# Kernel tuning notes

Hardware: AMD Instinct MI355X
Metric: run time of the kernel (lower is better)

The kernel has to match this reference:

```python
import jax, jax.numpy as jnp
import numpy as np

T, B, D, H = 512, 256, 256, 256  # seq_len, batch, input_dim, hidden_dim == n_qubits


def setup_inputs() -> dict:
    key = jax.random.key(0)
    k1, k2, k3 = jax.random.split(key, 3)
    inputs = jax.random.normal(k1, (T, B, D), dtype=jnp.float32)
    # stacked gate linears: order [forget, input, update, output]
    W = jax.random.normal(k2, (4, H, D + H), dtype=jnp.float32) * 0.05
    b = jax.random.normal(k3, (4, H), dtype=jnp.float32) * 0.05
    return {"inputs": inputs, "W": W, "b": b}


def reference(inputs, W, b):
    # Quantum gate with mean_field=True reduces exactly to cos(.):
    # |0> --RX(x)--> <Z> = cos(x); RZ layers are diagonal in Z and leave <Z> unchanged.
    batch = inputs.shape[1]
    h0 = jnp.zeros((batch, H), dtype=inputs.dtype)
    c0 = jnp.zeros((batch, H), dtype=inputs.dtype)

    def step(carry, x_t):
        h, c = carry
        comb = jnp.concatenate([x_t, h], axis=1)            # [B, D+H]
        z = jnp.einsum('gqd,bd->gbq', W, comb) + b[:, None, :]  # [4, B, H]
        f = jax.nn.sigmoid(jnp.cos(z[0]))
        i = jax.nn.sigmoid(jnp.cos(z[1]))
        g = jnp.tanh(jnp.cos(z[2]))
        o = jax.nn.sigmoid(jnp.cos(z[3]))
        c_new = f * c + i * g
        h_new = o * jnp.tanh(c_new)
        return (h_new, c_new), h_new

    (h_last, c_last), outputs = jax.lax.scan(step, (h0, c0), inputs)
    return outputs, h_last, c_last
```

## Files before the change

### kernel.cpp

```cpp
#include <hip/hip_runtime.h>

#define T_ 512
#define B_ 256
#define D_ 256
#define H_ 256

typedef short s16x8 __attribute__((ext_vector_type(8)));
typedef float f32x4 __attribute__((ext_vector_type(4)));

static __device__ __forceinline__ unsigned short f2bf(float f){
  unsigned u = __float_as_uint(f);
  u += 0x7FFFu + ((u >> 16) & 1u);
  return (unsigned short)(u >> 16);
}
static __device__ __forceinline__ float bf2f(unsigned short h){
  return __uint_as_float(((unsigned)h) << 16);
}
static __device__ __forceinline__ unsigned pk2(float a, float b){
  return (unsigned)f2bf(a) | ((unsigned)f2bf(b) << 16);
}
static __device__ __forceinline__ float sigf(float x){
  return __builtin_amdgcn_rcpf(1.0f + __expf(-x));
}
static __device__ __forceinline__ float tanhf_(float x){
  return 1.0f - 2.0f * __builtin_amdgcn_rcpf(__expf(2.0f * x) + 1.0f);
}

__global__ void k_cast(const float* __restrict__ W,
                       unsigned short* __restrict__ Wxb,
                       unsigned short* __restrict__ Whb)
{
  const int i = blockIdx.x * 256 + threadIdx.x;
  const int row = i >> 8;
  const int k = i & 255;
  Wxb[i] = f2bf(W[(size_t)row * 512 + k]);
  Whb[i] = f2bf(W[(size_t)row * 512 + 256 + k]);
}

__global__ void k_cast_x(const float* __restrict__ x,
                         unsigned short* __restrict__ xb)
{
  const size_t i = ((size_t)blockIdx.x * 256 + threadIdx.x) * 8;
  const float4 a = *(const float4*)(x + i);
  const float4 b = *(const float4*)(x + i + 4);
  uint4 w;
  w.x = pk2(a.x, a.y);  w.y = pk2(a.z, a.w);
  w.z = pk2(b.x, b.y);  w.w = pk2(b.z, b.w);
  *(uint4*)(xb + i) = w;
}

__global__ __launch_bounds__(512, 2) void k_phase1(
    const unsigned short* __restrict__ Wxb,
    const unsigned short* __restrict__ xb,
    const float* __restrict__ bias,
    unsigned short* __restrict__ zxf,
    int t0)
{
  extern __shared__ char smem[];
  char* Bs = smem + 65536;
  const int tid  = threadIdx.x;
  const int lane = tid & 63;
  const int wid  = tid >> 6;
  const int r16  = lane >> 4;
  const int c16  = lane & 15;
  const int wm = wid >> 2;
  const int wn = wid & 3;
  const int mbase  = blockIdx.y * 128;
  const int ntile0 = blockIdx.x * 16;
  const size_t nbase = (size_t)t0 * 256 + (size_t)ntile0 * 128;

#pragma unroll
  for (int r = 0; r < 8; ++r){
    const int ch = r * 512 + tid;
    const int row = ch >> 5;
    const int cc = ch & 31;
    uint4 v = *(const uint4*)(Wxb + (size_t)(mbase + row) * 256 + cc * 8);
    *(uint4*)(smem + row * 512 + ((cc * 16) ^ ((row & 7) << 4))) = v;
  }
  float bv[4][4];
#pragma unroll
  for (int mt = 0; mt < 4; ++mt)
#pragma unroll
    for (int i = 0; i < 4; ++i)
      bv[mt][i] = bias[mbase + wm * 64 + mt * 16 + r16 * 4 + i];

  uint4 pb[8];
#pragma unroll
  for (int r = 0; r < 8; ++r){
    const int ch = r * 512 + tid;
    const int row = ch >> 5;
    const int cc = ch & 31;
    pb[r] = *(const uint4*)(xb + (nbase + row) * 256 + cc * 8);
  }

  for (int it = 0; it < 16; ++it){
    __syncthreads();
#pragma unroll
    for (int r = 0; r < 8; ++r){
      const int ch = r * 512 + tid;
      const int row = ch >> 5;
      const int cc = ch & 31;
      *(uint4*)(Bs + row * 512 + ((cc * 16) ^ ((row & 7) << 4))) = pb[r];
    }
    __syncthreads();
    if (it < 15){
      const size_t nb = nbase + (size_t)(it + 1) * 128;
#pragma unroll
      for (int r = 0; r < 8; ++r){
        const int ch = r * 512 + tid;
        const int row = ch >> 5;
        const int cc = ch & 31;
        pb[r] = *(const uint4*)(xb + (nb + row) * 256 + cc * 8);
      }
    }

    f32x4 acc[4][2];
#pragma unroll
    for (int mt = 0; mt < 4; ++mt)
#pragma unroll
      for (int i = 0; i < 4; ++i){
        acc[mt][0][i] = bv[mt][i];
        acc[mt][1][i] = bv[mt][i];
      }

#pragma unroll
    for (int kc = 0; kc < 8; ++kc){
      s16x8 bf[2];
#pragma unroll
      for (int nt = 0; nt < 2; ++nt){
        const int row = wn * 32 + nt * 16 + c16;
        bf[nt] = *(const s16x8*)(Bs + row * 512 + ((kc * 64 + r16 * 16) ^ ((row & 7) << 4)));
      }
#pragma unroll
      for (int mt = 0; mt < 4; ++mt){
        const int row = wm * 64 + mt * 16 + c16;
        const s16x8 af = *(const s16x8*)(smem + row * 512 + ((kc * 64 + r16 * 16) ^ ((row & 7) << 4)));
#pragma unroll
        for (int nt = 0; nt < 2; ++nt)
          acc[mt][nt] = __builtin_amdgcn_mfma_f32_16x16x32_bf16(af, bf[nt], acc[mt][nt], 0, 0, 0);
      }
    }

    const int ntile = ntile0 + it;
#pragma unroll
    for (int mt = 0; mt < 4; ++mt)
#pragma unroll
      for (int ss = 0; ss < 2; ++ss){
        const int m16 = (mbase >> 4) + wm * 4 + mt;
        const size_t n16 = (size_t)ntile * 8 + wn * 2 + ss;
        uint2 p;
        p.x = pk2(acc[mt][ss][0], acc[mt][ss][1]);
        p.y = pk2(acc[mt][ss][2], acc[mt][ss][3]);
        *(uint2*)((char*)zxf + (n16 * 64 + m16) * 512 + lane * 8) = p;
      }
  }
}

__global__ __launch_bounds__(512, 2) void k_phase2(
    const unsigned short* __restrict__ Whb,
    const unsigned short* __restrict__ zxf,
    float* __restrict__ out,
    unsigned short* __restrict__ sh,
    float* __restrict__ sc,
    int t0, int TC)
{
  extern __shared__ char smem[];
  const int tid  = threadIdx.x;
  const int lane = tid & 63;
  const int wid  = tid >> 6;
  const int r16  = lane >> 4;
  const int c16  = lane & 15;
  const int bt   = blockIdx.x;
  const int b    = bt * 16 + c16;

  s16x8 wf[6][8];
#pragma unroll
  for (int g = 0; g < 3; ++g)
#pragma unroll
    for (int s = 0; s < 2; ++s){
      const int row = (g * 16 + wid * 2 + s) * 16 + c16;
      const unsigned short* wp = Whb + (size_t)row * 256 + r16 * 8;
#pragma unroll
      for (int kc = 0; kc < 8; ++kc)
        wf[g * 2 + s][kc] = *(const s16x8*)(wp + kc * 32);
    }
#pragma unroll
  for (int s = 0; s < 2; ++s){
    const int rt = 48 + wid * 2 + s;
#pragma unroll
    for (int r = 0; r < 8; ++r){
      const int ch = r * 64 + lane;
      const int rr = ch >> 5;
      const int cc = ch & 31;
      uint4 v = *(const uint4*)(Whb + (size_t)(rt * 16 + rr) * 256 + cc * 8);
      *(uint4*)(smem + (wid * 2 + s) * 8192 + rr * 512 + ((cc * 16) ^ ((rr & 7) << 4))) = v;
    }
  }

  float cst[2][4];
  char* hb0 = smem + 131072;
  if (t0 == 0){
#pragma unroll
    for (int s = 0; s < 2; ++s)
#pragma unroll
      for (int i = 0; i < 4; ++i) cst[s][i] = 0.0f;
    *(uint4*)(hb0 + tid * 16) = make_uint4(0, 0, 0, 0);
  } else {
#pragma unroll
    for (int s = 0; s < 2; ++s){
      const int q0 = (wid * 2 + s) * 16 + r16 * 4;
      const float4 cv = *(const float4*)(sc + (size_t)b * 256 + q0);
      cst[s][0] = cv.x; cst[s][1] = cv.y; cst[s][2] = cv.z; cst[s][3] = cv.w;
    }
    const int brow = tid >> 5;
    const int cc = tid & 31;
    uint4 v = *(const uint4*)((const char*)sh + (size_t)(bt * 16 + brow) * 512 + cc * 16);
    *(uint4*)(hb0 + brow * 512 + ((cc * 16) ^ ((brow & 7) << 4))) = v;
  }
  __syncthreads();

  const char* zlane = (const char*)zxf + (size_t)lane * 8;
  uint2 zc[2][4];
#pragma unroll
  for (int s = 0; s < 2; ++s)
#pragma unroll
    for (int g = 0; g < 4; ++g)
      zc[s][g] = *(const uint2*)(zlane + ((size_t)bt * 64 + g * 16 + wid * 2 + s) * 512);

  for (int t = t0; t < t0 + TC; ++t){
    const int tt = t - t0;
    const char* hread = smem + 131072 + ((tt & 1) << 13);
    char*      hwrite = smem + 131072 + (((tt & 1) ^ 1) << 13);
    const int ttn = (tt + 1 < TC) ? (tt + 1) : tt;
    const size_t znoff = ((size_t)ttn * 16 + bt) * 64 * 512;
    uint2 zn[2][4];

#pragma unroll
    for (int s = 0; s < 2; ++s){
      f32x4 acc[4];
#pragma unroll
      for (int g = 0; g < 4; ++g){
        acc[g][0] = bf2f((unsigned short)(zc[s][g].x & 0xFFFFu));
        acc[g][1] = bf2f((unsigned short)(zc[s][g].x >> 16));
        acc[g][2] = bf2f((unsigned short)(zc[s][g].y & 0xFFFFu));
        acc[g][3] = bf2f((unsigned short)(zc[s][g].y >> 16));
      }
#pragma unroll
      for (int g = 0; g < 4; ++g)
        zn[s][g] = *(const uint2*)(zlane + znoff + (size_t)(g * 16 + wid * 2 + s) * 512);

#pragma unroll
      for (int kc = 0; kc < 8; ++kc){
        const s16x8 hv = *(const s16x8*)(hread + c16 * 512 + ((kc * 64 + r16 * 16) ^ ((c16 & 7) << 4)));
        acc[0] = __builtin_amdgcn_mfma_f32_16x16x32_bf16(wf[0 + s][kc], hv, acc[0], 0, 0, 0);
        acc[1] = __builtin_amdgcn_mfma_f32_16x16x32_bf16(wf[2 + s][kc], hv, acc[1], 0, 0, 0);
        acc[2] = __builtin_amdgcn_mfma_f32_16x16x32_bf16(wf[4 + s][kc], hv, acc[2], 0, 0, 0);
        const s16x8 av = *(const s16x8*)(smem + (wid * 2 + s) * 8192 + c16 * 512 +
                                         ((kc * 64 + r16 * 16) ^ ((c16 & 7) << 4)));
        acc[3] = __builtin_amdgcn_mfma_f32_16x16x32_bf16(av, hv, acc[3], 0, 0, 0);
      }
      const int q0 = (wid * 2 + s) * 16 + r16 * 4;
      float ho[4];
#pragma unroll
      for (int i = 0; i < 4; ++i){
        const float fg = sigf(__cosf(acc[0][i]));
        const float ig = sigf(__cosf(acc[1][i]));
        const float gg = tanhf_(__cosf(acc[2][i]));
        const float og = sigf(__cosf(acc[3][i]));
        const float cn = fg * cst[s][i] + ig * gg;
        cst[s][i] = cn;
        ho[i] = og * tanhf_(cn);
      }
      *(float4*)(out + ((size_t)t * B_ + b) * H_ + q0) = make_float4(ho[0], ho[1], ho[2], ho[3]);
      *(uint2*)(hwrite + c16 * 512 + ((q0 * 2) ^ ((c16 & 7) << 4))) =
          make_uint2(pk2(ho[0], ho[1]), pk2(ho[2], ho[3]));
      if (t == T_ - 1){
        float* hl = out + (size_t)T_ * B_ * H_;
        *(float4*)(hl + (size_t)b * H_ + q0) = make_float4(ho[0], ho[1], ho[2], ho[3]);
        float* cl = hl + (size_t)B_ * H_;
        *(float4*)(cl + (size_t)b * H_ + q0) = make_float4(cst[s][0], cst[s][1], cst[s][2], cst[s][3]);
      }
    }
    __syncthreads();
#pragma unroll
    for (int s = 0; s < 2; ++s)
#pragma unroll
      for (int g = 0; g < 4; ++g)
        zc[s][g] = zn[s][g];
  }

  if (t0 + TC < T_){
    const char* hlast = smem + 131072 + (((((TC - 1) & 1)) ^ 1) << 13);
#pragma unroll
    for (int s = 0; s < 2; ++s){
      const int q0 = (wid * 2 + s) * 16 + r16 * 4;
      const uint2 hp = *(const uint2*)(hlast + c16 * 512 + ((q0 * 2) ^ ((c16 & 7) << 4)));
      *(uint2*)((char*)sh + (size_t)b * 512 + q0 * 2) = hp;
      *(float4*)(sc + (size_t)b * 256 + q0) = make_float4(cst[s][0], cst[s][1], cst[s][2], cst[s][3]);
    }
  }
}

extern "C" void kernel_launch(void* const* d_in, const int* in_sizes, int n_in,
                              void* d_out, int out_size, void* d_ws, size_t ws_size,
                              hipStream_t stream)
{
  const float* x    = (const float*)d_in[0];
  const float* W    = (const float*)d_in[1];
  const float* bias = (const float*)d_in[2];
  float* out = (float*)d_out;

  char* ws = (char*)d_ws;
  unsigned short* Wxb = (unsigned short*)(ws);
  unsigned short* Whb = (unsigned short*)(ws + 524288);
  unsigned short* sh  = (unsigned short*)(ws + 1048576);
  float*          sc  = (float*)(ws + 1179648);
  unsigned short* xb  = (unsigned short*)(ws + 1441792);
  const unsigned long long zx_off = 1441792ull + (unsigned long long)T_ * B_ * D_ * 2ull;
  unsigned short* zxf = (unsigned short*)(ws + zx_off);

  (void)hipFuncSetAttribute((const void*)k_phase1, hipFuncAttributeMaxDynamicSharedMemorySize, 131072);
  (void)hipFuncSetAttribute((const void*)k_phase2, hipFuncAttributeMaxDynamicSharedMemorySize, 147456);

  int TC = 8;
  const int cands[6] = {512, 256, 128, 64, 32, 16};
  for (int i = 0; i < 6; ++i){
    if (zx_off + (unsigned long long)cands[i] * 524288ull <= (unsigned long long)ws_size){
      TC = cands[i];
      break;
    }
  }

  k_cast<<<1024, 256, 0, stream>>>(W, Wxb, Whb);
  k_cast_x<<<(T_ * B_ * D_) / 2048, 256, 0, stream>>>(x, xb);
  for (int t0 = 0; t0 < T_; t0 += TC){
    k_phase1<<<dim3(TC / 8, 8, 1), 512, 131072, stream>>>(Wxb, xb, bias, zxf, t0);
    k_phase2<<<dim3(16, 1, 1), 512, 147456, stream>>>(Whb, zxf, out, sh, sc, t0, TC);
  }
}
```

Measured before the change: 2.916 ms.

## Split recurrent phase across paired workgroups with global-memory h exchange

The recurrent kernel now launches two workgroups per batch tile, each owning half of the hidden units. All four gate weight slices sit in registers, so the large LDS weight buffer is gone. Each step, the halves exchange their new h slices through a global buffer and synchronise with release/acquire flags and a spin-wait. This doubles the CUs working on the serial recurrence and halves the MFMA work per step. In exchange it adds a cross-workgroup global-memory handshake to every timestep, and progress relies on both paired workgroups being resident at the same time.

```diff
diff --git a/kernel.cpp b/kernel.cpp
--- a/kernel.cpp
+++ b/kernel.cpp
@@ -162,6 +162,8 @@
     float* __restrict__ out,
     unsigned short* __restrict__ sh,
     float* __restrict__ sc,
+    unsigned short* __restrict__ hx,
+    int* __restrict__ flags,
     int t0, int TC)
 {
   extern __shared__ char smem[];
@@ -170,134 +172,124 @@
   const int wid  = tid >> 6;
   const int r16  = lane >> 4;
   const int c16  = lane & 15;
-  const int bt   = blockIdx.x;
+  const int bt   = blockIdx.x >> 1;
+  const int half = blockIdx.x & 1;
   const int b    = bt * 16 + c16;
-
-  s16x8 wf[6][8];
-#pragma unroll
-  for (int g = 0; g < 3; ++g)
-#pragma unroll
-    for (int s = 0; s < 2; ++s){
-      const int row = (g * 16 + wid * 2 + s) * 16 + c16;
-      const unsigned short* wp = Whb + (size_t)row * 256 + r16 * 8;
-#pragma unroll
-      for (int kc = 0; kc < 8; ++kc)
-        wf[g * 2 + s][kc] = *(const s16x8*)(wp + kc * 32);
-    }
-#pragma unroll
-  for (int s = 0; s < 2; ++s){
-    const int rt = 48 + wid * 2 + s;
-#pragma unroll
-    for (int r = 0; r < 8; ++r){
-      const int ch = r * 64 + lane;
-      const int rr = ch >> 5;
-      const int cc = ch & 31;
-      uint4 v = *(const uint4*)(Whb + (size_t)(rt * 16 + rr) * 256 + cc * 8);
-      *(uint4*)(smem + (wid * 2 + s) * 8192 + rr * 512 + ((cc * 16) ^ ((rr & 7) << 4))) = v;
-    }
-  }
-
-  float cst[2][4];
-  char* hb0 = smem + 131072;
+  const int q    = half * 128 + wid * 16 + r16 * 4;
+
+  s16x8 wf[4][8];
+#pragma unroll
+  for (int g = 0; g < 4; ++g){
+    const int row = (g * 16 + half * 8 + wid) * 16 + c16;
+    const unsigned short* wp = Whb + (size_t)row * 256 + r16 * 8;
+#pragma unroll
+    for (int kc = 0; kc < 8; ++kc)
+      wf[g][kc] = *(const s16x8*)(wp + kc * 32);
+  }
+
+  float cst[4];
   if (t0 == 0){
 #pragma unroll
-    for (int s = 0; s < 2; ++s)
-#pragma unroll
-      for (int i = 0; i < 4; ++i) cst[s][i] = 0.0f;
-    *(uint4*)(hb0 + tid * 16) = make_uint4(0, 0, 0, 0);
+    for (int i = 0; i < 4; ++i) cst[i] = 0.0f;
+    *(uint4*)(smem + tid * 16) = make_uint4(0, 0, 0, 0);
   } else {
-#pragma unroll
-    for (int s = 0; s < 2; ++s){
-      const int q0 = (wid * 2 + s) * 16 + r16 * 4;
-      const float4 cv = *(const float4*)(sc + (size_t)b * 256 + q0);
-      cst[s][0] = cv.x; cst[s][1] = cv.y; cst[s][2] = cv.z; cst[s][3] = cv.w;
-    }
-    const int brow = tid >> 5;
-    const int cc = tid & 31;
-    uint4 v = *(const uint4*)((const char*)sh + (size_t)(bt * 16 + brow) * 512 + cc * 16);
-    *(uint4*)(hb0 + brow * 512 + ((cc * 16) ^ ((brow & 7) << 4))) = v;
+    const float4 cv = *(const float4*)(sc + (size_t)b * 256 + q);
+    cst[0] = cv.x; cst[1] = cv.y; cst[2] = cv.z; cst[3] = cv.w;
+    const int b2 = tid & 15;
+    const int qq = (tid >> 4) * 8;
+    uint4 v = *(const uint4*)(sh + (size_t)(bt * 16 + b2) * 256 + qq);
+    *(uint4*)(smem + ((t0 & 1) << 13) + b2 * 512 + ((qq * 2) ^ ((b2 & 7) << 4))) = v;
   }
   __syncthreads();
 
   const char* zlane = (const char*)zxf + (size_t)lane * 8;
-  uint2 zc[2][4];
-#pragma unroll
-  for (int s = 0; s < 2; ++s)
-#pragma unroll
-    for (int g = 0; g < 4; ++g)
-      zc[s][g] = *(const uint2*)(zlane + ((size_t)bt * 64 + g * 16 + wid * 2 + s) * 512);
+  const int mt0 = half * 8 + wid;
+  uint2 zc[4], zn[4];
+#pragma unroll
+  for (int g = 0; g < 4; ++g)
+    zc[g] = *(const uint2*)(zlane + ((size_t)bt * 64 + g * 16 + mt0) * 512);
+
+  uint2 hkeep;
+  const int qg = wid * 4 + r16;
 
   for (int t = t0; t < t0 + TC; ++t){
     const int tt = t - t0;
-    const char* hread = smem + 131072 + ((tt & 1) << 13);
-    char*      hwrite = smem + 131072 + (((tt & 1) ^ 1) << 13);
+    const char* hread = smem + ((t & 1) << 13);
+    char*      hwrite = smem + (((t & 1) ^ 1) << 13);
     const int ttn = (tt + 1 < TC) ? (tt + 1) : tt;
-    const size_t znoff = ((size_t)ttn * 16 + bt) * 64 * 512;
-    uint2 zn[2][4];
-
-#pragma unroll
-    for (int s = 0; s < 2; ++s){
-      f32x4 acc[4];
-#pragma unroll
-      for (int g = 0; g < 4; ++g){
-        acc[g][0] = bf2f((unsigned short)(zc[s][g].x & 0xFFFFu));
-        acc[g][1] = bf2f((unsigned short)(zc[s][g].x >> 16));
-        acc[g][2] = bf2f((unsigned short)(zc[s][g].y & 0xFFFFu));
-        acc[g][3] = bf2f((unsigned short)(zc[s][g].y >> 16));
-      }
-#pragma unroll
-      for (int g = 0; g < 4; ++g)
-        zn[s][g] = *(const uint2*)(zlane + znoff + (size_t)(g * 16 + wid * 2 + s) * 512);
-
-#pragma unroll
-      for (int kc = 0; kc < 8; ++kc){
-        const s16x8 hv = *(const s16x8*)(hread + c16 * 512 + ((kc * 64 + r16 * 16) ^ ((c16 & 7) << 4)));
-        acc[0] = __builtin_amdgcn_mfma_f32_16x16x32_bf16(wf[0 + s][kc], hv, acc[0], 0, 0, 0);
-        acc[1] = __builtin_amdgcn_mfma_f32_16x16x32_bf16(wf[2 + s][kc], hv, acc[1], 0, 0, 0);
-        acc[2] = __builtin_amdgcn_mfma_f32_16x16x32_bf16(wf[4 + s][kc], hv, acc[2], 0, 0, 0);
-        const s16x8 av = *(const s16x8*)(smem + (wid * 2 + s) * 8192 + c16 * 512 +
-                                         ((kc * 64 + r16 * 16) ^ ((c16 & 7) << 4)));
-        acc[3] = __builtin_amdgcn_mfma_f32_16x16x32_bf16(av, hv, acc[3], 0, 0, 0);
-      }
-      const int q0 = (wid * 2 + s) * 16 + r16 * 4;
-      float ho[4];
-#pragma unroll
-      for (int i = 0; i < 4; ++i){
-        const float fg = sigf(__cosf(acc[0][i]));
-        const float ig = sigf(__cosf(acc[1][i]));
-        const float gg = tanhf_(__cosf(acc[2][i]));
-        const float og = sigf(__cosf(acc[3][i]));
-        const float cn = fg * cst[s][i] + ig * gg;
-        cst[s][i] = cn;
-        ho[i] = og * tanhf_(cn);
-      }
-      *(float4*)(out + ((size_t)t * B_ + b) * H_ + q0) = make_float4(ho[0], ho[1], ho[2], ho[3]);
-      *(uint2*)(hwrite + c16 * 512 + ((q0 * 2) ^ ((c16 & 7) << 4))) =
-          make_uint2(pk2(ho[0], ho[1]), pk2(ho[2], ho[3]));
-      if (t == T_ - 1){
-        float* hl = out + (size_t)T_ * B_ * H_;
-        *(float4*)(hl + (size_t)b * H_ + q0) = make_float4(ho[0], ho[1], ho[2], ho[3]);
-        float* cl = hl + (size_t)B_ * H_;
-        *(float4*)(cl + (size_t)b * H_ + q0) = make_float4(cst[s][0], cst[s][1], cst[s][2], cst[s][3]);
-      }
-    }
-    __syncthreads();
-#pragma unroll
-    for (int s = 0; s < 2; ++s)
-#pragma unroll
-      for (int g = 0; g < 4; ++g)
-        zc[s][g] = zn[s][g];
+
+#pragma unroll
+    for (int g = 0; g < 4; ++g)
+      zn[g] = *(const uint2*)(zlane + (((size_t)ttn * 16 + bt) * 64 + g * 16 + mt0) * 512);
+
+    f32x4 acc[4];
+#pragma unroll
+    for (int g = 0; g < 4; ++g){
+      acc[g][0] = bf2f((unsigned short)(zc[g].x & 0xFFFFu));
+      acc[g][1] = bf2f((unsigned short)(zc[g].x >> 16));
+      acc[g][2] = bf2f((unsigned short)(zc[g].y & 0xFFFFu));
+      acc[g][3] = bf2f((unsigned short)(zc[g].y >> 16));
+    }
+
+#pragma unroll
+    for (int kc = 0; kc < 8; ++kc){
+      const s16x8 hv = *(const s16x8*)(hread + c16 * 512 + ((kc * 64 + r16 * 16) ^ ((c16 & 7) << 4)));
+      acc[0] = __builtin_amdgcn_mfma_f32_16x16x32_bf16(wf[0][kc], hv, acc[0], 0, 0, 0);
+      acc[1] = __builtin_amdgcn_mfma_f32_16x16x32_bf16(wf[1][kc], hv, acc[1], 0, 0, 0);
+      acc[2] = __builtin_amdgcn_mfma_f32_16x16x32_bf16(wf[2][kc], hv, acc[2], 0, 0, 0);
+      acc[3] = __builtin_amdgcn_mfma_f32_16x16x32_bf16(wf[3][kc], hv, acc[3], 0, 0, 0);
+    }
+
+    float ho[4];
+#pragma unroll
+    for (int i = 0; i < 4; ++i){
+      const float fg = sigf(__cosf(acc[0][i]));
+      const float ig = sigf(__cosf(acc[1][i]));
+      const float gg = tanhf_(__cosf(acc[2][i]));
+      const float og = sigf(__cosf(acc[3][i]));
+      const float cn = fg * cst[i] + ig * gg;
+      cst[i] = cn;
+      ho[i] = og * tanhf_(cn);
+    }
+    *(float4*)(out + ((size_t)t * B_ + b) * H_ + q) = make_float4(ho[0], ho[1], ho[2], ho[3]);
+    hkeep = make_uint2(pk2(ho[0], ho[1]), pk2(ho[2], ho[3]));
+    *(uint2*)(hwrite + c16 * 512 + ((q * 2) ^ ((c16 & 7) << 4))) = hkeep;
+    if (t == T_ - 1){
+      float* hl = out + (size_t)T_ * B_ * H_;
+      *(float4*)(hl + (size_t)b * H_ + q) = make_float4(ho[0], ho[1], ho[2], ho[3]);
+      float* cl = hl + (size_t)B_ * H_;
+      *(float4*)(cl + (size_t)b * H_ + q) = make_float4(cst[0], cst[1], cst[2], cst[3]);
+    } else {
+      const size_t slot = ((((size_t)((t + 1) & 1) * 16 + bt) * 2 + half) * 32 + qg) * 16 + c16;
+      *(uint2*)(hx + slot * 4) = hkeep;
+    }
+
+    asm volatile("s_waitcnt vmcnt(0)" ::: "memory");
+    __builtin_amdgcn_s_barrier();
+
+    if (t < T_ - 1){
+      if (tid == 0)
+        __hip_atomic_store(&flags[(bt * 2 + half) * 16], t + 1,
+                           __ATOMIC_RELEASE, __HIP_MEMORY_SCOPE_AGENT);
+      const int* pf = &flags[(bt * 2 + (half ^ 1)) * 16];
+      while (__hip_atomic_load(pf, __ATOMIC_ACQUIRE, __HIP_MEMORY_SCOPE_AGENT) < t + 1) { }
+      const int b2 = tid & 15;
+      const int qg2 = tid >> 4;
+      const size_t pslot = ((((size_t)((t + 1) & 1) * 16 + bt) * 2 + (half ^ 1)) * 32 + qg2) * 16 + b2;
+      const uint2 pv = *(const uint2*)(hx + pslot * 4);
+      const int qp = (half ^ 1) * 128 + qg2 * 4;
+      *(uint2*)(hwrite + b2 * 512 + ((qp * 2) ^ ((b2 & 7) << 4))) = pv;
+    }
+    asm volatile("s_waitcnt lgkmcnt(0)" ::: "memory");
+    __builtin_amdgcn_s_barrier();
+
+#pragma unroll
+    for (int g = 0; g < 4; ++g) zc[g] = zn[g];
   }
 
   if (t0 + TC < T_){
-    const char* hlast = smem + 131072 + (((((TC - 1) & 1)) ^ 1) << 13);
-#pragma unroll
-    for (int s = 0; s < 2; ++s){
-      const int q0 = (wid * 2 + s) * 16 + r16 * 4;
-      const uint2 hp = *(const uint2*)(hlast + c16 * 512 + ((q0 * 2) ^ ((c16 & 7) << 4)));
-      *(uint2*)((char*)sh + (size_t)b * 512 + q0 * 2) = hp;
-      *(float4*)(sc + (size_t)b * 256 + q0) = make_float4(cst[s][0], cst[s][1], cst[s][2], cst[s][3]);
-    }
+    *(uint2*)(sh + (size_t)b * 256 + q) = hkeep;
+    *(float4*)(sc + (size_t)b * 256 + q) = make_float4(cst[0], cst[1], cst[2], cst[3]);
   }
 }
 
@@ -311,16 +303,18 @@
   float* out = (float*)d_out;
 
   char* ws = (char*)d_ws;
-  unsigned short* Wxb = (unsigned short*)(ws);
-  unsigned short* Whb = (unsigned short*)(ws + 524288);
-  unsigned short* sh  = (unsigned short*)(ws + 1048576);
-  float*          sc  = (float*)(ws + 1179648);
-  unsigned short* xb  = (unsigned short*)(ws + 1441792);
-  const unsigned long long zx_off = 1441792ull + (unsigned long long)T_ * B_ * D_ * 2ull;
-  unsigned short* zxf = (unsigned short*)(ws + zx_off);
+  unsigned short* Wxb  = (unsigned short*)(ws);
+  unsigned short* Whb  = (unsigned short*)(ws + 524288);
+  unsigned short* sh   = (unsigned short*)(ws + 1048576);
+  float*          sc   = (float*)(ws + 1179648);
+  int*            flags= (int*)(ws + 1441792);
+  unsigned short* hx   = (unsigned short*)(ws + 1445888);
+  unsigned short* xb   = (unsigned short*)(ws + 1708032);
+  const unsigned long long zx_off = 1708032ull + (unsigned long long)T_ * B_ * D_ * 2ull;
+  unsigned short* zxf  = (unsigned short*)(ws + zx_off);
 
   (void)hipFuncSetAttribute((const void*)k_phase1, hipFuncAttributeMaxDynamicSharedMemorySize, 131072);
-  (void)hipFuncSetAttribute((const void*)k_phase2, hipFuncAttributeMaxDynamicSharedMemorySize, 147456);
+  (void)hipFuncSetAttribute((const void*)k_phase2, hipFuncAttributeMaxDynamicSharedMemorySize, 16384);
 
   int TC = 8;
   const int cands[6] = {512, 256, 128, 64, 32, 16};
@@ -331,10 +325,11 @@
     }
   }
 
+  (void)hipMemsetAsync(flags, 0, 4096, stream);
   k_cast<<<1024, 256, 0, stream>>>(W, Wxb, Whb);
   k_cast_x<<<(T_ * B_ * D_) / 2048, 256, 0, stream>>>(x, xb);
   for (int t0 = 0; t0 < T_; t0 += TC){
     k_phase1<<<dim3(TC / 8, 8, 1), 512, 131072, stream>>>(Wxb, xb, bias, zxf, t0);
-    k_phase2<<<dim3(16, 1, 1), 512, 147456, stream>>>(Whb, zxf, out, sh, sc, t0, TC);
-  }
-}
+    k_phase2<<<dim3(32, 1, 1), 512, 16384, stream>>>(Whb, zxf, out, sh, sc, hx, flags, t0, TC);
+  }
+}
```

Measured after the change: 3.187 ms. 1.09x slower.

## Pre-swizzle bf16 weights and inputs into MFMA fragment order during cast

Applied to the files above, without the earlier changes.

The cast kernels now write Wx, Wh and x in bf16 laid out in MFMA fragment order (16-row tiles, kc-major, lane-contiguous). Phase1 and phase2 can then copy straight to LDS and read fragments at lane*16 offsets with no XOR swizzle or row/column index math. The register fragments for Wh also load as contiguous chunks. Phase2 keeps the last packed h in registers, so the final LDS read-back for the carry is dropped, and the bf16 unpack uses a cheaper shift/mask. The risk is that LDS bank conflicts, previously avoided by the swizzle, now depend entirely on the linear fragment layout.

```diff
diff --git a/kernel.cpp b/kernel.cpp
--- a/kernel.cpp
+++ b/kernel.cpp
@@ -7,18 +7,22 @@
 
 typedef short s16x8 __attribute__((ext_vector_type(8)));
 typedef float f32x4 __attribute__((ext_vector_type(4)));
-
-static __device__ __forceinline__ unsigned short f2bf(float f){
+typedef unsigned short u16;
+
+static __device__ __forceinline__ u16 f2bf(float f){
   unsigned u = __float_as_uint(f);
   u += 0x7FFFu + ((u >> 16) & 1u);
-  return (unsigned short)(u >> 16);
-}
-static __device__ __forceinline__ float bf2f(unsigned short h){
-  return __uint_as_float(((unsigned)h) << 16);
+  return (u16)(u >> 16);
 }
 static __device__ __forceinline__ unsigned pk2(float a, float b){
   return (unsigned)f2bf(a) | ((unsigned)f2bf(b) << 16);
 }
+static __device__ __forceinline__ float bflo(unsigned u){
+  return __uint_as_float(u << 16);
+}
+static __device__ __forceinline__ float bfhi(unsigned u){
+  return __uint_as_float(u & 0xFFFF0000u);
+}
 static __device__ __forceinline__ float sigf(float x){
   return __builtin_amdgcn_rcpf(1.0f + __expf(-x));
 }
@@ -26,35 +30,48 @@
   return 1.0f - 2.0f * __builtin_amdgcn_rcpf(__expf(2.0f * x) + 1.0f);
 }
 
+
 __global__ void k_cast(const float* __restrict__ W,
-                       unsigned short* __restrict__ Wxb,
-                       unsigned short* __restrict__ Whb)
-{
-  const int i = blockIdx.x * 256 + threadIdx.x;
-  const int row = i >> 8;
-  const int k = i & 255;
-  Wxb[i] = f2bf(W[(size_t)row * 512 + k]);
-  Whb[i] = f2bf(W[(size_t)row * 512 + 256 + k]);
-}
-
-__global__ void k_cast_x(const float* __restrict__ x,
-                         unsigned short* __restrict__ xb)
-{
-  const size_t i = ((size_t)blockIdx.x * 256 + threadIdx.x) * 8;
-  const float4 a = *(const float4*)(x + i);
-  const float4 b = *(const float4*)(x + i + 4);
+                       u16* __restrict__ Wxb, u16* __restrict__ Whb)
+{
+  const int i   = blockIdx.x * 256 + threadIdx.x;
+  const int m   = i >> 15;
+  const int idx = i & 32767;
+  const int c16 = idx & 15;
+  const int r16 = (idx >> 4) & 3;
+  const int kc  = (idx >> 6) & 7;
+  const int t16 = idx >> 9;
+  const int row = t16 * 16 + c16;
+  const int k   = kc * 32 + r16 * 8;
+  const float* src = W + (size_t)row * 512 + (m ? 256 + k : k);
+  const float4 a = *(const float4*)src;
+  const float4 b = *(const float4*)(src + 4);
   uint4 w;
   w.x = pk2(a.x, a.y);  w.y = pk2(a.z, a.w);
   w.z = pk2(b.x, b.y);  w.w = pk2(b.z, b.w);
-  *(uint4*)(xb + i) = w;
+  u16* dst = m ? Whb : Wxb;
+  *(uint4*)(dst + (size_t)idx * 8) = w;
+}
+
+__global__ void k_cast_x(const float* __restrict__ x, u16* __restrict__ xb)
+{
+  const size_t i = (size_t)blockIdx.x * 256 + threadIdx.x;
+  const int c16 = (int)(i & 15);
+  const int r16 = (int)(i >> 4) & 3;
+  const int kc  = (int)(i >> 6) & 7;
+  const size_t n16 = i >> 9;
+  const float* src = x + (n16 * 16 + c16) * 256 + kc * 32 + r16 * 8;
+  const float4 a = *(const float4*)src;
+  const float4 b = *(const float4*)(src + 4);
+  uint4 w;
+  w.x = pk2(a.x, a.y);  w.y = pk2(a.z, a.w);
+  w.z = pk2(b.x, b.y);  w.w = pk2(b.z, b.w);
+  *(uint4*)(xb + i * 8) = w;
 }
 
 __global__ __launch_bounds__(512, 2) void k_phase1(
-    const unsigned short* __restrict__ Wxb,
-    const unsigned short* __restrict__ xb,
-    const float* __restrict__ bias,
-    unsigned short* __restrict__ zxf,
-    int t0)
+    const u16* __restrict__ Wxb, const u16* __restrict__ xb,
+    const float* __restrict__ bias, u16* __restrict__ zxf, int t0)
 {
   extern __shared__ char smem[];
   char* Bs = smem + 65536;
@@ -62,56 +79,46 @@
   const int lane = tid & 63;
   const int wid  = tid >> 6;
   const int r16  = lane >> 4;
-  const int c16  = lane & 15;
-  const int wm = wid >> 2;
-  const int wn = wid & 3;
-  const int mbase  = blockIdx.y * 128;
-  const int ntile0 = blockIdx.x * 16;
-  const size_t nbase = (size_t)t0 * 256 + (size_t)ntile0 * 128;
+  const int wm   = wid >> 2;
+  const int wn   = wid & 3;
+  const char* WxC = (const char*)Wxb;
+  const char* xbC = (const char*)xb;
+  char* zxC = (char*)zxf;
+
+  const size_t abase = (size_t)blockIdx.y << 16;
+  const size_t nbase = ((size_t)t0 * 16 + (size_t)blockIdx.x * 128) << 13;
 
 #pragma unroll
   for (int r = 0; r < 8; ++r){
-    const int ch = r * 512 + tid;
-    const int row = ch >> 5;
-    const int cc = ch & 31;
-    uint4 v = *(const uint4*)(Wxb + (size_t)(mbase + row) * 256 + cc * 8);
-    *(uint4*)(smem + row * 512 + ((cc * 16) ^ ((row & 7) << 4))) = v;
+    const int o = (r * 512 + tid) * 16;
+    *(uint4*)(smem + o) = *(const uint4*)(WxC + abase + o);
   }
   float bv[4][4];
 #pragma unroll
   for (int mt = 0; mt < 4; ++mt)
 #pragma unroll
     for (int i = 0; i < 4; ++i)
-      bv[mt][i] = bias[mbase + wm * 64 + mt * 16 + r16 * 4 + i];
+      bv[mt][i] = bias[blockIdx.y * 128 + wm * 64 + mt * 16 + r16 * 4 + i];
 
   uint4 pb[8];
 #pragma unroll
-  for (int r = 0; r < 8; ++r){
-    const int ch = r * 512 + tid;
-    const int row = ch >> 5;
-    const int cc = ch & 31;
-    pb[r] = *(const uint4*)(xb + (nbase + row) * 256 + cc * 8);
-  }
+  for (int r = 0; r < 8; ++r)
+    pb[r] = *(const uint4*)(xbC + nbase + (r * 512 + tid) * 16);
+
+  __syncthreads();
 
   for (int it = 0; it < 16; ++it){
+    if (it) __syncthreads();
+#pragma unroll
+    for (int r = 0; r < 8; ++r)
+      *(uint4*)(Bs + (r * 512 + tid) * 16) = pb[r];
     __syncthreads();
-#pragma unroll
-    for (int r = 0; r < 8; ++r){
-      const int ch = r * 512 + tid;
-      const int row = ch >> 5;
-      const int cc = ch & 31;
-      *(uint4*)(Bs + row * 512 + ((cc * 16) ^ ((row & 7) << 4))) = pb[r];
-    }
-    __syncthreads();
+
     if (it < 15){
-      const size_t nb = nbase + (size_t)(it + 1) * 128;
-#pragma unroll
-      for (int r = 0; r < 8; ++r){
-        const int ch = r * 512 + tid;
-        const int row = ch >> 5;
-        const int cc = ch & 31;
-        pb[r] = *(const uint4*)(xb + (nb + row) * 256 + cc * 8);
-      }
+      const size_t nb = nbase + (size_t)(it + 1) * 65536;
+#pragma unroll
+      for (int r = 0; r < 8; ++r)
+        pb[r] = *(const uint4*)(xbC + nb + (r * 512 + tid) * 16);
     }
 
     f32x4 acc[4][2];
@@ -125,43 +132,33 @@
 
 #pragma unroll
     for (int kc = 0; kc < 8; ++kc){
-      s16x8 bf[2];
+      const s16x8 bf0 = *(const s16x8*)(Bs + ((wn * 2 + 0) << 13) + (kc << 10) + lane * 16);
+      const s16x8 bf1 = *(const s16x8*)(Bs + ((wn * 2 + 1) << 13) + (kc << 10) + lane * 16);
+#pragma unroll
+      for (int mt = 0; mt < 4; ++mt){
+        const s16x8 af = *(const s16x8*)(smem + ((wm * 4 + mt) << 13) + (kc << 10) + lane * 16);
+        acc[mt][0] = __builtin_amdgcn_mfma_f32_16x16x32_bf16(af, bf0, acc[mt][0], 0, 0, 0);
+        acc[mt][1] = __builtin_amdgcn_mfma_f32_16x16x32_bf16(af, bf1, acc[mt][1], 0, 0, 0);
+      }
+    }
+
+#pragma unroll
+    for (int mt = 0; mt < 4; ++mt)
 #pragma unroll
       for (int nt = 0; nt < 2; ++nt){
-        const int row = wn * 32 + nt * 16 + c16;
-        bf[nt] = *(const s16x8*)(Bs + row * 512 + ((kc * 64 + r16 * 16) ^ ((row & 7) << 4)));
-      }
-#pragma unroll
-      for (int mt = 0; mt < 4; ++mt){
-        const int row = wm * 64 + mt * 16 + c16;
-        const s16x8 af = *(const s16x8*)(smem + row * 512 + ((kc * 64 + r16 * 16) ^ ((row & 7) << 4)));
-#pragma unroll
-        for (int nt = 0; nt < 2; ++nt)
-          acc[mt][nt] = __builtin_amdgcn_mfma_f32_16x16x32_bf16(af, bf[nt], acc[mt][nt], 0, 0, 0);
-      }
-    }
-
-    const int ntile = ntile0 + it;
-#pragma unroll
-    for (int mt = 0; mt < 4; ++mt)
-#pragma unroll
-      for (int ss = 0; ss < 2; ++ss){
-        const int m16 = (mbase >> 4) + wm * 4 + mt;
-        const size_t n16 = (size_t)ntile * 8 + wn * 2 + ss;
+        const size_t n16l = (size_t)blockIdx.x * 128 + it * 8 + wn * 2 + nt;
+        const int   m16g  = blockIdx.y * 8 + wm * 4 + mt;
         uint2 p;
-        p.x = pk2(acc[mt][ss][0], acc[mt][ss][1]);
-        p.y = pk2(acc[mt][ss][2], acc[mt][ss][3]);
-        *(uint2*)((char*)zxf + (n16 * 64 + m16) * 512 + lane * 8) = p;
+        p.x = pk2(acc[mt][nt][0], acc[mt][nt][1]);
+        p.y = pk2(acc[mt][nt][2], acc[mt][nt][3]);
+        *(uint2*)(zxC + (n16l * 64 + m16g) * 512 + lane * 8) = p;
       }
   }
 }
 
 __global__ __launch_bounds__(512, 2) void k_phase2(
-    const unsigned short* __restrict__ Whb,
-    const unsigned short* __restrict__ zxf,
-    float* __restrict__ out,
-    unsigned short* __restrict__ sh,
-    float* __restrict__ sc,
+    const u16* __restrict__ Whb, const u16* __restrict__ zxf,
+    float* __restrict__ out, u16* __restrict__ sh, float* __restrict__ sc,
     int t0, int TC)
 {
   extern __shared__ char smem[];
@@ -172,29 +169,22 @@
   const int c16  = lane & 15;
   const int bt   = blockIdx.x;
   const int b    = bt * 16 + c16;
+  const char* WhC = (const char*)Whb;
 
   s16x8 wf[6][8];
 #pragma unroll
   for (int g = 0; g < 3; ++g)
 #pragma unroll
-    for (int s = 0; s < 2; ++s){
-      const int row = (g * 16 + wid * 2 + s) * 16 + c16;
-      const unsigned short* wp = Whb + (size_t)row * 256 + r16 * 8;
+    for (int s = 0; s < 2; ++s)
 #pragma unroll
       for (int kc = 0; kc < 8; ++kc)
-        wf[g * 2 + s][kc] = *(const s16x8*)(wp + kc * 32);
-    }
-#pragma unroll
-  for (int s = 0; s < 2; ++s){
-    const int rt = 48 + wid * 2 + s;
-#pragma unroll
-    for (int r = 0; r < 8; ++r){
-      const int ch = r * 64 + lane;
-      const int rr = ch >> 5;
-      const int cc = ch & 31;
-      uint4 v = *(const uint4*)(Whb + (size_t)(rt * 16 + rr) * 256 + cc * 8);
-      *(uint4*)(smem + (wid * 2 + s) * 8192 + rr * 512 + ((cc * 16) ^ ((rr & 7) << 4))) = v;
-    }
+        wf[g * 2 + s][kc] =
+            *(const s16x8*)(WhC + ((g * 16 + wid * 2 + s) << 13) + (kc << 10) + lane * 16);
+
+#pragma unroll
+  for (int r = 0; r < 16; ++r){
+    const int o = (r * 512 + tid) * 16;
+    *(uint4*)(smem + o) = *(const uint4*)(WhC + (48 << 13) + o);
   }
 
   float cst[2][4];
@@ -226,6 +216,8 @@
 #pragma unroll
     for (int g = 0; g < 4; ++g)
       zc[s][g] = *(const uint2*)(zlane + ((size_t)bt * 64 + g * 16 + wid * 2 + s) * 512);
+
+  unsigned hpack[2][2];
 
   for (int t = t0; t < t0 + TC; ++t){
     const int tt = t - t0;
@@ -240,10 +232,10 @@
       f32x4 acc[4];
 #pragma unroll
       for (int g = 0; g < 4; ++g){
-        acc[g][0] = bf2f((unsigned short)(zc[s][g].x & 0xFFFFu));
-        acc[g][1] = bf2f((unsigned short)(zc[s][g].x >> 16));
-        acc[g][2] = bf2f((unsigned short)(zc[s][g].y & 0xFFFFu));
-        acc[g][3] = bf2f((unsigned short)(zc[s][g].y >> 16));
+        acc[g][0] = bflo(zc[s][g].x);
+        acc[g][1] = bfhi(zc[s][g].x);
+        acc[g][2] = bflo(zc[s][g].y);
+        acc[g][3] = bfhi(zc[s][g].y);
       }
 #pragma unroll
       for (int g = 0; g < 4; ++g)
@@ -255,8 +247,7 @@
         acc[0] = __builtin_amdgcn_mfma_f32_16x16x32_bf16(wf[0 + s][kc], hv, acc[0], 0, 0, 0);
         acc[1] = __builtin_amdgcn_mfma_f32_16x16x32_bf16(wf[2 + s][kc], hv, acc[1], 0, 0, 0);
         acc[2] = __builtin_amdgcn_mfma_f32_16x16x32_bf16(wf[4 + s][kc], hv, acc[2], 0, 0, 0);
-        const s16x8 av = *(const s16x8*)(smem + (wid * 2 + s) * 8192 + c16 * 512 +
-                                         ((kc * 64 + r16 * 16) ^ ((c16 & 7) << 4)));
+        const s16x8 av = *(const s16x8*)(smem + ((wid * 2 + s) << 13) + (kc << 10) + lane * 16);
         acc[3] = __builtin_amdgcn_mfma_f32_16x16x32_bf16(av, hv, acc[3], 0, 0, 0);
       }
       const int q0 = (wid * 2 + s) * 16 + r16 * 4;
@@ -272,8 +263,10 @@
         ho[i] = og * tanhf_(cn);
       }
       *(float4*)(out + ((size_t)t * B_ + b) * H_ + q0) = make_float4(ho[0], ho[1], ho[2], ho[3]);
+      hpack[s][0] = pk2(ho[0], ho[1]);
+      hpack[s][1] = pk2(ho[2], ho[3]);
       *(uint2*)(hwrite + c16 * 512 + ((q0 * 2) ^ ((c16 & 7) << 4))) =
-          make_uint2(pk2(ho[0], ho[1]), pk2(ho[2], ho[3]));
+          make_uint2(hpack[s][0], hpack[s][1]);
       if (t == T_ - 1){
         float* hl = out + (size_t)T_ * B_ * H_;
         *(float4*)(hl + (size_t)b * H_ + q0) = make_float4(ho[0], ho[1], ho[2], ho[3]);
@@ -290,12 +283,10 @@
   }
 
   if (t0 + TC < T_){
-    const char* hlast = smem + 131072 + (((((TC - 1) & 1)) ^ 1) << 13);
 #pragma unroll
     for (int s = 0; s < 2; ++s){
       const int q0 = (wid * 2 + s) * 16 + r16 * 4;
-      const uint2 hp = *(const uint2*)(hlast + c16 * 512 + ((q0 * 2) ^ ((c16 & 7) << 4)));
-      *(uint2*)((char*)sh + (size_t)b * 512 + q0 * 2) = hp;
+      *(uint2*)((char*)sh + (size_t)b * 512 + q0 * 2) = make_uint2(hpack[s][0], hpack[s][1]);
       *(float4*)(sc + (size_t)b * 256 + q0) = make_float4(cst[s][0], cst[s][1], cst[s][2], cst[s][3]);
     }
   }
@@ -311,30 +302,30 @@
   float* out = (float*)d_out;
 
   char* ws = (char*)d_ws;
-  unsigned short* Wxb = (unsigned short*)(ws);
-  unsigned short* Whb = (unsigned short*)(ws + 524288);
-  unsigned short* sh  = (unsigned short*)(ws + 1048576);
-  float*          sc  = (float*)(ws + 1179648);
-  unsigned short* xb  = (unsigned short*)(ws + 1441792);
+  u16*   Wxb = (u16*)(ws);
+  u16*   Whb = (u16*)(ws + 524288);
+  u16*   sh  = (u16*)(ws + 1048576);
+  float* sc  = (float*)(ws + 1179648);
+  u16*   xb  = (u16*)(ws + 1441792);
   const unsigned long long zx_off = 1441792ull + (unsigned long long)T_ * B_ * D_ * 2ull;
-  unsigned short* zxf = (unsigned short*)(ws + zx_off);
+  u16*   zxf = (u16*)(ws + zx_off);
 
   (void)hipFuncSetAttribute((const void*)k_phase1, hipFuncAttributeMaxDynamicSharedMemorySize, 131072);
   (void)hipFuncSetAttribute((const void*)k_phase2, hipFuncAttributeMaxDynamicSharedMemorySize, 147456);
 
   int TC = 8;
-  const int cands[6] = {512, 256, 128, 64, 32, 16};
-  for (int i = 0; i < 6; ++i){
+  const int cands[7] = {512, 256, 128, 64, 32, 16, 8};
+  for (int i = 0; i < 7; ++i){
     if (zx_off + (unsigned long long)cands[i] * 524288ull <= (unsigned long long)ws_size){
       TC = cands[i];
       break;
     }
   }
 
-  k_cast<<<1024, 256, 0, stream>>>(W, Wxb, Whb);
-  k_cast_x<<<(T_ * B_ * D_) / 2048, 256, 0, stream>>>(x, xb);
+  k_cast<<<256, 256, 0, stream>>>(W, Wxb, Whb);
+  k_cast_x<<<16384, 256, 0, stream>>>(x, xb);
   for (int t0 = 0; t0 < T_; t0 += TC){
-    k_phase1<<<dim3(TC / 8, 8, 1), 512, 131072, stream>>>(Wxb, xb, bias, zxf, t0);
+    k_phase1<<<dim3((TC + 7) / 8, 8, 1), 512, 131072, stream>>>(Wxb, xb, bias, zxf, t0);
     k_phase2<<<dim3(16, 1, 1), 512, 147456, stream>>>(Whb, zxf, out, sh, sc, t0, TC);
   }
 }
```

After: 2.581 ms. 1.13x faster.
